# Kernel tuning notes

Measured on AMD Instinct MI355X. Metric: run time of the kernel, lower is better.

Reference implementation:

```python
import jax, jax.numpy as jnp
import numpy as np

B, S, D_IN, D_OUT = 4, 2048, 1024, 1024


def setup_inputs() -> dict:
    key = jax.random.key(0)
    k1, k2, k3, k4 = jax.random.split(key, 4)
    x = jax.random.normal(k1, (B, S, D_IN), dtype=jnp.float32)
    scale = 1.0 / np.sqrt(D_IN)
    Wq = jax.random.normal(k2, (D_IN, D_OUT), dtype=jnp.float32) * scale
    Wk = jax.random.normal(k3, (D_IN, D_OUT), dtype=jnp.float32) * scale
    Wv = jax.random.normal(k4, (D_IN, D_OUT), dtype=jnp.float32) * scale
    return {"x": x, "Wq": Wq, "Wk": Wk, "Wv": Wv}


def reference(x, Wq, Wk, Wv):
    # QKV projections (Linear, no bias)
    q = jnp.einsum('bsd,de->bse', x, Wq)  # [B,S,D_OUT]
    k = jnp.einsum('bsd,de->bse', x, Wk)
    v = jnp.einsum('bsd,de->bse', x, Wv)
    d_out = Wq.shape[1]
    # raw scores [B,S,S], scaled after masking (identical math: -inf stays -inf)
    scores = jnp.einsum('bqe,bke->bqk', q, k) * (d_out ** -0.5)
    S_ = x.shape[1]
    # causal mask: future positions (j > i) are masked out
    causal = jnp.triu(jnp.ones((S_, S_), dtype=bool), k=1)
    scores = jnp.where(causal[None, :, :], -jnp.inf, scores)
    attn = jax.nn.softmax(scores, axis=-1)  # dropout p=0.0 -> identity
    return jnp.einsum('bqk,bke->bqe', attn, v)
```

## Files before the change

kernel.cpp:

```cpp
#include <hip/hip_runtime.h>
#include <stdint.h>

typedef unsigned short u16;
typedef unsigned int u32;
typedef __bf16 bf16x8 __attribute__((ext_vector_type(8)));
typedef float f32x4 __attribute__((ext_vector_type(4)));

#define BM 128
#define BN 128
#define BK 64

__device__ __forceinline__ u16 f2bf(float x) {
  union { float f; uint32_t u; } c; c.f = x;
  uint32_t r = (c.u + 0x7FFFu + ((c.u >> 16) & 1u)) >> 16;
  return (u16)r;
}

__device__ __forceinline__ void async_copy16(const u16* g, u16* l) {
  __builtin_amdgcn_global_load_lds(
      (const __attribute__((address_space(1))) void*)g,
      (__attribute__((address_space(3))) void*)l,
      16, 0, 0);
}

__global__ void flag_init(u32* __restrict__ f) { if (threadIdx.x == 0) *f = 0; }

__global__ void detect_dtype(const u16* __restrict__ w, u32* __restrict__ cnt) {
  int i = blockIdx.x * 256 + threadIdx.x;
  if ((w[i] & 0x7F80u) == 0x7F80u) atomicAdd(cnt, 1u);
}

__global__ __launch_bounds__(256)
void normalize_x(const void* __restrict__ src, u16* __restrict__ dst,
                 const u32* __restrict__ flag, long n) {
  long i = ((long)blockIdx.x * 256 + threadIdx.x) * 8;
  if (i >= n) return;
  u16 o[8];
  if (*flag > 32) {
    const float* s = (const float*)src + i;
    f32x4 a = *(const f32x4*)s;
    f32x4 b = *(const f32x4*)(s + 4);
#pragma unroll
    for (int c = 0; c < 4; ++c) { o[c] = f2bf(a[c]); o[c + 4] = f2bf(b[c]); }
  } else {
    *(uint4*)o = *(const uint4*)((const u16*)src + i);
  }
  *(uint4*)(dst + i) = *(uint4*)o;
}

__global__ void zerofill_u16(u16* __restrict__ p) {
  long i = (long)blockIdx.x * 256 + threadIdx.x;
  p[i] = 0;
}

__global__ __launch_bounds__(256)
void transnorm_w(const void* __restrict__ s0, const void* __restrict__ s1,
                 const void* __restrict__ s2, u16* __restrict__ dst,
                 const u32* __restrict__ flag, int Dd)
{
  __shared__ u16 tile[64][72];
  const int z = blockIdx.z;
  const void* src = (z == 0) ? s0 : (z == 1) ? s1 : s2;
  u16* out = dst + (long)z * Dd * Dd;
  const int r0 = blockIdx.y * 64, c0 = blockIdx.x * 64;
  const int tid = threadIdx.x;
  const bool isf32 = (*flag > 32);
#pragma unroll
  for (int p = 0; p < 2; ++p) {
    int v = tid + p * 256;
    int row = v >> 3, c8 = (v & 7) * 8;
    u16 t[8];
    if (isf32) {
      const float* sp = (const float*)src + (long)(r0 + row) * Dd + c0 + c8;
      f32x4 a = *(const f32x4*)sp;
      f32x4 b = *(const f32x4*)(sp + 4);
#pragma unroll
      for (int c = 0; c < 4; ++c) { t[c] = f2bf(a[c]); t[c + 4] = f2bf(b[c]); }
    } else {
      *(uint4*)t = *(const uint4*)((const u16*)src + (long)(r0 + row) * Dd + c0 + c8);
    }
#pragma unroll
    for (int c = 0; c < 8; ++c) tile[row][c8 + c] = t[c];
  }
  __syncthreads();
#pragma unroll
  for (int p = 0; p < 2; ++p) {
    int v = tid + p * 256;
    int oc = v >> 3, r8 = (v & 7) * 8;
    union { uint4 q; u16 s[8]; } t;
#pragma unroll
    for (int c = 0; c < 8; ++c) t.s[c] = tile[r8 + c][oc];
    *(uint4*)(out + (long)(c0 + oc) * Dd + r0 + r8) = t.q;
  }
}

template <int MODE>
__global__ __launch_bounds__(256, 2)
void gemm_nt(const u16* __restrict__ A, const u16* __restrict__ B, void* __restrict__ Cv,
             const u32* __restrict__ flag,
             int K, int lda, int ldb, int ldc,
             long sA, long sB, long sC, long cOff,
             float scale, int causal, int trik)
{
  int bm = blockIdx.y;
  if (trik) bm = gridDim.y - 1 - bm;
  const int bn = blockIdx.x, bz = blockIdx.z;
  if (causal && bn > bm) return;

  __shared__ u16 As[BM * BK];
  __shared__ u16 Bs[BN * BK];

  A += (long)bz * sA;
  B += (long)bz * sB;

  const int tid  = threadIdx.x;
  const int wid  = tid >> 6;
  const int lane = tid & 63;
  const int l16  = lane & 15;
  const int lk   = lane >> 4;
  const int srow = lane >> 3;
  const int swz  = ((lane & 7) ^ srow) * 8;
  const int m0 = bm * BM, n0 = bn * BN;

  int nk = K / BK;
  if (trik) { int lim = (m0 + BM) / BK; if (lim < nk) nk = lim; }

  f32x4 acc[4][4] = {};

  for (int kt = 0; kt < nk; ++kt) {
    const int k0 = kt * BK;
#pragma unroll
    for (int c = 0; c < 4; ++c) {
      const int rb = wid * 32 + c * 8;
      async_copy16(A + (long)(m0 + rb + srow) * lda + (k0 + swz), As + rb * BK);
      async_copy16(B + (long)(n0 + rb + srow) * ldb + (k0 + swz), Bs + rb * BK);
    }
    __syncthreads();
#pragma unroll
    for (int kh = 0; kh < 2; ++kh) {
      bf16x8 av[4], bv[4];
#pragma unroll
      for (int i = 0; i < 4; ++i) {
        const int Ra = (wid >> 1) * 64 + i * 16 + l16;
        const int Rb = (wid & 1)  * 64 + i * 16 + l16;
        const int ca = ((kh * 4 + lk) ^ (l16 & 7)) * 8;
        av[i] = *(const bf16x8*)(As + Ra * BK + ca);
        bv[i] = *(const bf16x8*)(Bs + Rb * BK + ca);
      }
#pragma unroll
      for (int mi = 0; mi < 4; ++mi)
#pragma unroll
        for (int ni = 0; ni < 4; ++ni)
          acc[mi][ni] = __builtin_amdgcn_mfma_f32_16x16x32_bf16(av[mi], bv[ni], acc[mi][ni], 0, 0, 0);
    }
    __syncthreads();
  }

  const int rb0 = m0 + (wid >> 1) * 64;
  const int cb0 = n0 + (wid & 1) * 64;
  const long cbase = (long)bz * sC + cOff;
  const bool f32out = (MODE == 1) || (MODE == 2 && *flag > 32);

#pragma unroll
  for (int mi = 0; mi < 4; ++mi)
#pragma unroll
    for (int ni = 0; ni < 4; ++ni) {
      const int row = rb0 + mi * 16 + lk * 4;
      const int col = cb0 + ni * 16 + l16;
#pragma unroll
      for (int r = 0; r < 4; ++r) {
        const float v = acc[mi][ni][r] * scale;
        const long idx = cbase + (long)(row + r) * ldc + col;
        if constexpr (MODE == 0) {
          ((u16*)Cv)[idx] = f2bf(v);
        } else if constexpr (MODE == 1) {
          ((float*)Cv)[idx] = v;
        } else {
          if (f32out) ((float*)Cv)[idx] = v;
          else        ((u16*)Cv)[idx]   = f2bf(v);
        }
      }
    }
}

__global__ __launch_bounds__(256)
void transpose_bf16(const u16* __restrict__ in, u16* __restrict__ out,
                    int ldIn, int ldOut, long sIn, long sOut)
{
  __shared__ u16 tile[64][72];
  const int bz = blockIdx.z;
  in  += (long)bz * sIn;
  out += (long)bz * sOut;
  const int r0 = blockIdx.y * 64, c0 = blockIdx.x * 64;
  const int tid = threadIdx.x;
#pragma unroll
  for (int p = 0; p < 2; ++p) {
    int v = tid + p * 256;
    int row = v >> 3, c8 = (v & 7) * 8;
    union { uint4 q; u16 s[8]; } t;
    t.q = *(const uint4*)(in + (long)(r0 + row) * ldIn + c0 + c8);
#pragma unroll
    for (int i = 0; i < 8; ++i) tile[row][c8 + i] = t.s[i];
  }
  __syncthreads();
#pragma unroll
  for (int p = 0; p < 2; ++p) {
    int v = tid + p * 256;
    int oc = v >> 3, r8 = (v & 7) * 8;
    union { uint4 q; u16 s[8]; } t;
#pragma unroll
    for (int i = 0; i < 8; ++i) t.s[i] = tile[r8 + i][oc];
    *(uint4*)(out + (long)(c0 + oc) * ldOut + r0 + r8) = t.q;
  }
}

__global__ __launch_bounds__(256)
void softmax_causal(char* __restrict__ base, long rowStrideB, int modS)
{
  const long r = blockIdx.x;
  const int i = (int)(r % modS);
  float* sc = (float*)(base + r * rowStrideB);
  u16*   pr = (u16*)(base + r * rowStrideB);
  const int n = i + 1;
  const int tid = threadIdx.x;
  const int j0 = tid * 8;
  const int wv = tid >> 6, lane = tid & 63;
  __shared__ float red[4];

  float e[8];
  float m = -3.0e38f;
  if (j0 < n) {
    f32x4 a = *(const f32x4*)(sc + j0);
    f32x4 b = *(const f32x4*)(sc + j0 + 4);
#pragma unroll
    for (int c = 0; c < 4; ++c) { e[c] = a[c]; e[c + 4] = b[c]; }
#pragma unroll
    for (int c = 0; c < 8; ++c) {
      if (j0 + c < n) m = fmaxf(m, e[c]); else e[c] = -3.0e38f;
    }
  } else {
#pragma unroll
    for (int c = 0; c < 8; ++c) e[c] = -3.0e38f;
  }
#pragma unroll
  for (int o = 32; o > 0; o >>= 1) m = fmaxf(m, __shfl_xor(m, o));
  if (lane == 0) red[wv] = m;
  __syncthreads();
  m = fmaxf(fmaxf(red[0], red[1]), fmaxf(red[2], red[3]));
  __syncthreads();

  float s = 0.f;
#pragma unroll
  for (int c = 0; c < 8; ++c) { float x = __expf(e[c] - m); e[c] = x; s += x; }
#pragma unroll
  for (int o = 32; o > 0; o >>= 1) s += __shfl_xor(s, o);
  if (lane == 0) red[wv] = s;
  __syncthreads();
  s = red[0] + red[1] + red[2] + red[3];
  const float inv = 1.0f / s;

  u16 o8[8];
#pragma unroll
  for (int c = 0; c < 8; ++c) o8[c] = f2bf(e[c] * inv);
  *(uint4*)(pr + j0) = *(uint4*)o8;
}

extern "C" void kernel_launch(void* const* d_in, const int* in_sizes, int n_in,
                              void* d_out, int out_size, void* d_ws, size_t ws_size,
                              hipStream_t stream)
{
  (void)in_sizes; (void)n_in; (void)out_size;
  const int Bb = 4, S = 2048, D = 1024, D3 = 3072;
  const long SD = (long)S * D;
  const long SS = (long)S * S;
  const long N_X = (long)Bb * SD;
  const long N_W = (long)D * D;

  char* ws = (char*)d_ws;
  size_t off = 0;
  auto take = [&](size_t bytes) -> void* {
    void* p = ws + off;
    off = (off + bytes + 255) & ~((size_t)255);
    return p;
  };

  u32* flag = (u32*)take(4096);
  u16* xn   = (u16*)take((size_t)N_X * 2);
  u16* WT3  = (u16*)take((size_t)3 * N_W * 2);
  const size_t off_common = off;

  const size_t needA = off_common + (size_t)(N_X * 3 * 2)
                     + (size_t)(N_X * 2)
                     + (size_t)(Bb * SS * 4) + 4096;
  const size_t needC = off_common + (size_t)(S * (long)D3 * 2)
                     + (size_t)(SD * 2)
                     + (size_t)(SS * 4) + 4096;

  if (ws_size < needC) {
    zerofill_u16<<<(int)(N_X / 256), 256, 0, stream>>>((u16*)d_out);
    return;
  }

  flag_init<<<1, 64, 0, stream>>>(flag);
  detect_dtype<<<1024, 256, 0, stream>>>((const u16*)d_in[1], flag);

  normalize_x<<<(int)(N_X / 2048), 256, 0, stream>>>(d_in[0], xn, flag, N_X);
  transnorm_w<<<dim3(D / 64, D / 64, 3), 256, 0, stream>>>(
      d_in[1], d_in[2], d_in[3], WT3, flag, D);

  const float scl = 0.03125f;

  if (ws_size >= needA) {
    u16*   QKV = (u16*)take((size_t)N_X * 3 * 2);
    u16*   VT  = (u16*)take((size_t)N_X * 2);
    float* sc  = (float*)take((size_t)Bb * SS * 4);

    gemm_nt<0><<<dim3(D3 / BN, (int)(N_X / D) / BM, 1), 256, 0, stream>>>(
        xn, WT3, QKV, flag, D, D, D, D3, 0, 0, 0, 0, 1.f, 0, 0);

    transpose_bf16<<<dim3(D / 64, S / 64, Bb), 256, 0, stream>>>(
        QKV + 2048, VT, D3, S, (long)S * D3, SD);

    gemm_nt<1><<<dim3(S / BN, S / BM, Bb), 256, 0, stream>>>(
        QKV, QKV + 1024, sc, flag, D, D3, D3, S,
        (long)S * D3, (long)S * D3, SS, 0, scl, 1, 0);

    softmax_causal<<<Bb * S, 256, 0, stream>>>((char*)sc, (long)S * 4, S);

    gemm_nt<2><<<dim3(D / BN, S / BM, Bb), 256, 0, stream>>>(
        (u16*)sc, VT, d_out, flag, S, 2 * S, S, D,
        2 * SS, SD, SD, 0, 1.f, 0, 1);
  } else {
    u16*   QKVb = (u16*)take((size_t)S * D3 * 2);
    u16*   VTb  = (u16*)take((size_t)SD * 2);
    float* scb  = (float*)take((size_t)SS * 4);

    for (int b = 0; b < Bb; ++b) {
      gemm_nt<0><<<dim3(D3 / BN, S / BM, 1), 256, 0, stream>>>(
          xn + (long)b * SD, WT3, QKVb, flag, D, D, D, D3, 0, 0, 0, 0, 1.f, 0, 0);

      transpose_bf16<<<dim3(D / 64, S / 64, 1), 256, 0, stream>>>(
          QKVb + 2048, VTb, D3, S, 0, 0);

      gemm_nt<1><<<dim3(S / BN, S / BM, 1), 256, 0, stream>>>(
          QKVb, QKVb + 1024, scb, flag, D, D3, D3, S, 0, 0, 0, 0, scl, 1, 0);

      softmax_causal<<<S, 256, 0, stream>>>((char*)scb, (long)S * 4, S);

      gemm_nt<2><<<dim3(D / BN, S / BM, 1), 256, 0, stream>>>(
          (u16*)scb, VTb, d_out, flag, S, 2 * S, S, D,
          0, 0, 0, (long)b * SD, 1.f, 0, 1);
    }
  }
}
```

Measured before the change: 255.4 us.

## Fuse preprocessing kernels into one and switch GEMM to 32x32x16 MFMA

Merges the flag init, dtype detection, x conversion and weight transpose kernels into a single prep kernel. Each block detects the dtype itself by scanning the first 8192 halfwords of Wq, which removes three launches and the global atomic. Separately, the shared GEMM now uses 32x32x16 bf16 MFMA tiles instead of 16x16x32, which means fewer instructions and LDS reads per k-step. The costs are a redundant dtype scan in every block and a different accumulator register layout in the epilogue.

Result: slower. 267.7 us (+4.8%).

```diff
diff --git a/kernel.cpp b/kernel.cpp
--- a/kernel.cpp
+++ b/kernel.cpp
@@ -5,6 +5,7 @@
 typedef unsigned int u32;
 typedef __bf16 bf16x8 __attribute__((ext_vector_type(8)));
 typedef float f32x4 __attribute__((ext_vector_type(4)));
+typedef float f32x16 __attribute__((ext_vector_type(16)));
 
 #define BM 128
 #define BN 128
@@ -23,74 +24,82 @@
       16, 0, 0);
 }
 
-__global__ void flag_init(u32* __restrict__ f) { if (threadIdx.x == 0) *f = 0; }
-
-__global__ void detect_dtype(const u16* __restrict__ w, u32* __restrict__ cnt) {
-  int i = blockIdx.x * 256 + threadIdx.x;
-  if ((w[i] & 0x7F80u) == 0x7F80u) atomicAdd(cnt, 1u);
-}
-
-__global__ __launch_bounds__(256)
-void normalize_x(const void* __restrict__ src, u16* __restrict__ dst,
-                 const u32* __restrict__ flag, long n) {
-  long i = ((long)blockIdx.x * 256 + threadIdx.x) * 8;
-  if (i >= n) return;
-  u16 o[8];
-  if (*flag > 32) {
-    const float* s = (const float*)src + i;
-    f32x4 a = *(const f32x4*)s;
-    f32x4 b = *(const f32x4*)(s + 4);
-#pragma unroll
-    for (int c = 0; c < 4; ++c) { o[c] = f2bf(a[c]); o[c + 4] = f2bf(b[c]); }
-  } else {
-    *(uint4*)o = *(const uint4*)((const u16*)src + i);
-  }
-  *(uint4*)(dst + i) = *(uint4*)o;
-}
-
 __global__ void zerofill_u16(u16* __restrict__ p) {
   long i = (long)blockIdx.x * 256 + threadIdx.x;
   p[i] = 0;
 }
 
 __global__ __launch_bounds__(256)
-void transnorm_w(const void* __restrict__ s0, const void* __restrict__ s1,
-                 const void* __restrict__ s2, u16* __restrict__ dst,
-                 const u32* __restrict__ flag, int Dd)
-{
+void prep(const void* __restrict__ xs, const void* __restrict__ w0,
+          const void* __restrict__ w1, const void* __restrict__ w2,
+          u16* __restrict__ xn, u16* __restrict__ WT3, u32* __restrict__ flag,
+          int nxb)
+{
+  __shared__ int sh_hits;
   __shared__ u16 tile[64][72];
-  const int z = blockIdx.z;
-  const void* src = (z == 0) ? s0 : (z == 1) ? s1 : s2;
-  u16* out = dst + (long)z * Dd * Dd;
-  const int r0 = blockIdx.y * 64, c0 = blockIdx.x * 64;
+  if (threadIdx.x == 0) sh_hits = 0;
+  __syncthreads();
+  {
+    const u16* w = (const u16*)w0;
+    int h = 0;
+    for (int i = threadIdx.x; i < 8192; i += 256)
+      if ((w[i] & 0x7F80u) == 0x7F80u) h++;
+    if (h) atomicAdd(&sh_hits, h);
+  }
+  __syncthreads();
+  const bool isf32 = (sh_hits > 0);
+  const int blk = blockIdx.x;
   const int tid = threadIdx.x;
-  const bool isf32 = (*flag > 32);
-#pragma unroll
-  for (int p = 0; p < 2; ++p) {
-    int v = tid + p * 256;
-    int row = v >> 3, c8 = (v & 7) * 8;
-    u16 t[8];
+  if (blk == 0 && tid == 0) *flag = isf32 ? 1000u : 0u;
+
+  if (blk < nxb) {
+    long i = ((long)blk * 256 + tid) * 8;
+    u16 o[8];
     if (isf32) {
-      const float* sp = (const float*)src + (long)(r0 + row) * Dd + c0 + c8;
-      f32x4 a = *(const f32x4*)sp;
-      f32x4 b = *(const f32x4*)(sp + 4);
-#pragma unroll
-      for (int c = 0; c < 4; ++c) { t[c] = f2bf(a[c]); t[c + 4] = f2bf(b[c]); }
+      const float* s = (const float*)xs + i;
+      f32x4 a = *(const f32x4*)s;
+      f32x4 b = *(const f32x4*)(s + 4);
+#pragma unroll
+      for (int c = 0; c < 4; ++c) { o[c] = f2bf(a[c]); o[c + 4] = f2bf(b[c]); }
     } else {
-      *(uint4*)t = *(const uint4*)((const u16*)src + (long)(r0 + row) * Dd + c0 + c8);
-    }
-#pragma unroll
-    for (int c = 0; c < 8; ++c) tile[row][c8 + c] = t[c];
-  }
-  __syncthreads();
-#pragma unroll
-  for (int p = 0; p < 2; ++p) {
-    int v = tid + p * 256;
-    int oc = v >> 3, r8 = (v & 7) * 8;
-    union { uint4 q; u16 s[8]; } t;
-#pragma unroll
-    for (int c = 0; c < 8; ++c) t.s[c] = tile[r8 + c][oc];
-    *(uint4*)(out + (long)(c0 + oc) * Dd + r0 + r8) = t.q;
+      *(uint4*)o = *(const uint4*)((const u16*)xs + i);
+    }
+    *(uint4*)(xn + i) = *(uint4*)o;
+  } else {
+    const int Dd = 1024;
+    int t = blk - nxb;
+    int z = t >> 8;
+    int r = t & 255;
+    const int r0 = (r >> 4) * 64, c0 = (r & 15) * 64;
+    const void* src = (z == 0) ? w0 : (z == 1) ? w1 : w2;
+    u16* out = WT3 + (long)z * Dd * Dd;
+#pragma unroll
+    for (int p = 0; p < 2; ++p) {
+      int v = tid + p * 256;
+      int row = v >> 3, c8 = (v & 7) * 8;
+      u16 tt[8];
+      if (isf32) {
+        const float* sp = (const float*)src + (long)(r0 + row) * Dd + c0 + c8;
+        f32x4 a = *(const f32x4*)sp;
+        f32x4 b = *(const f32x4*)(sp + 4);
+#pragma unroll
+        for (int c = 0; c < 4; ++c) { tt[c] = f2bf(a[c]); tt[c + 4] = f2bf(b[c]); }
+      } else {
+        *(uint4*)tt = *(const uint4*)((const u16*)src + (long)(r0 + row) * Dd + c0 + c8);
+      }
+#pragma unroll
+      for (int c = 0; c < 8; ++c) tile[row][c8 + c] = tt[c];
+    }
+    __syncthreads();
+#pragma unroll
+    for (int p = 0; p < 2; ++p) {
+      int v = tid + p * 256;
+      int oc = v >> 3, r8 = (v & 7) * 8;
+      union { uint4 q; u16 s[8]; } tt;
+#pragma unroll
+      for (int c = 0; c < 8; ++c) tt.s[c] = tile[r8 + c][oc];
+      *(uint4*)(out + (long)(c0 + oc) * Dd + r0 + r8) = tt.q;
+    }
   }
 }
 
@@ -116,8 +125,8 @@
   const int tid  = threadIdx.x;
   const int wid  = tid >> 6;
   const int lane = tid & 63;
-  const int l16  = lane & 15;
-  const int lk   = lane >> 4;
+  const int l32  = lane & 31;
+  const int lh   = lane >> 5;
   const int srow = lane >> 3;
   const int swz  = ((lane & 7) ^ srow) * 8;
   const int m0 = bm * BM, n0 = bn * BN;
@@ -125,7 +134,7 @@
   int nk = K / BK;
   if (trik) { int lim = (m0 + BM) / BK; if (lim < nk) nk = lim; }
 
-  f32x4 acc[4][4] = {};
+  f32x16 acc[2][2] = {};
 
   for (int kt = 0; kt < nk; ++kt) {
     const int k0 = kt * BK;
@@ -137,21 +146,21 @@
     }
     __syncthreads();
 #pragma unroll
-    for (int kh = 0; kh < 2; ++kh) {
-      bf16x8 av[4], bv[4];
-#pragma unroll
-      for (int i = 0; i < 4; ++i) {
-        const int Ra = (wid >> 1) * 64 + i * 16 + l16;
-        const int Rb = (wid & 1)  * 64 + i * 16 + l16;
-        const int ca = ((kh * 4 + lk) ^ (l16 & 7)) * 8;
-        av[i] = *(const bf16x8*)(As + Ra * BK + ca);
-        bv[i] = *(const bf16x8*)(Bs + Rb * BK + ca);
+    for (int ks = 0; ks < 4; ++ks) {
+      bf16x8 av[2], bv[2];
+      const int cb = ((ks * 2 + lh) ^ (lane & 7)) * 8;
+#pragma unroll
+      for (int i = 0; i < 2; ++i) {
+        const int Ra = (wid >> 1) * 64 + i * 32 + l32;
+        const int Rb = (wid & 1)  * 64 + i * 32 + l32;
+        av[i] = *(const bf16x8*)(As + Ra * BK + cb);
+        bv[i] = *(const bf16x8*)(Bs + Rb * BK + cb);
       }
 #pragma unroll
-      for (int mi = 0; mi < 4; ++mi)
-#pragma unroll
-        for (int ni = 0; ni < 4; ++ni)
-          acc[mi][ni] = __builtin_amdgcn_mfma_f32_16x16x32_bf16(av[mi], bv[ni], acc[mi][ni], 0, 0, 0);
+      for (int mi = 0; mi < 2; ++mi)
+#pragma unroll
+        for (int ni = 0; ni < 2; ++ni)
+          acc[mi][ni] = __builtin_amdgcn_mfma_f32_32x32x16_bf16(av[mi], bv[ni], acc[mi][ni], 0, 0, 0);
     }
     __syncthreads();
   }
@@ -162,15 +171,15 @@
   const bool f32out = (MODE == 1) || (MODE == 2 && *flag > 32);
 
 #pragma unroll
-  for (int mi = 0; mi < 4; ++mi)
-#pragma unroll
-    for (int ni = 0; ni < 4; ++ni) {
-      const int row = rb0 + mi * 16 + lk * 4;
-      const int col = cb0 + ni * 16 + l16;
-#pragma unroll
-      for (int r = 0; r < 4; ++r) {
-        const float v = acc[mi][ni][r] * scale;
-        const long idx = cbase + (long)(row + r) * ldc + col;
+  for (int mi = 0; mi < 2; ++mi)
+#pragma unroll
+    for (int ni = 0; ni < 2; ++ni) {
+      const int col = cb0 + ni * 32 + l32;
+#pragma unroll
+      for (int reg = 0; reg < 16; ++reg) {
+        const int row = rb0 + mi * 32 + (reg & 3) + 8 * (reg >> 2) + 4 * lh;
+        const float v = acc[mi][ni][reg] * scale;
+        const long idx = cbase + (long)row * ldc + col;
         if constexpr (MODE == 0) {
           ((u16*)Cv)[idx] = f2bf(v);
         } else if constexpr (MODE == 1) {
@@ -301,12 +310,9 @@
     return;
   }
 
-  flag_init<<<1, 64, 0, stream>>>(flag);
-  detect_dtype<<<1024, 256, 0, stream>>>((const u16*)d_in[1], flag);
-
-  normalize_x<<<(int)(N_X / 2048), 256, 0, stream>>>(d_in[0], xn, flag, N_X);
-  transnorm_w<<<dim3(D / 64, D / 64, 3), 256, 0, stream>>>(
-      d_in[1], d_in[2], d_in[3], WT3, flag, D);
+  const int nxb = (int)(N_X / 2048);
+  prep<<<nxb + 768, 256, 0, stream>>>(d_in[0], d_in[1], d_in[2], d_in[3],
+                                      xn, WT3, flag, nxb);
 
   const float scl = 0.03125f;
 
```
